# Performance work log

Measured on AMD Instinct MI355X. Metric: run time of the kernel, lower is better.

## Reference

```python
import jax, jax.numpy as jnp
import numpy as np

N = 16_777_216
H, W = 239, 319            # shape=(320,240): H=shape[1]-1, W=shape[0]-1
TIME_DIV = 4               # group_num=8 // 2
PSH, PSW = 16, 16          # patch_size
PH, PW = (H + 1) // PSH, (W + 1) // PSW   # 15, 20
TOKEN_NUM = PH * PW        # 300
PATCH_SIZE = PSH * PSW     # 256
B = 1e-4
TOTAL = TIME_DIV * 2 * PATCH_SIZE * TOKEN_NUM  # index[0]*bins[0]


def setup_inputs() -> dict:
    key = jax.random.key(0)
    k1, k2, k3, k4 = jax.random.split(key, 4)
    # events: (t sorted ascending, x in [0,W), y in [0,H), polarity in {0,1})
    t = jnp.sort(jax.random.uniform(k1, (N,), minval=0.0, maxval=1e4))
    xs = jax.random.uniform(k2, (N,), minval=0.0, maxval=float(W))
    ys = jax.random.uniform(k3, (N,), minval=0.0, maxval=float(H))
    p = jax.random.randint(k4, (N,), 0, 2).astype(jnp.float32)
    x = jnp.stack([t, xs, ys, p], axis=1)  # [N, 4], no inf values
    return {"x": x}


def reference(x):
    # x: [N, 4] columns (t, x, y, polarity); assumed inf-free (torch filter is a no-op)
    w = (x[:, 3] != 2).astype(x.dtype)                       # polarity-valid weight
    t = x[:, 0]
    wt = (t - t[0]) / (t[-1] - t[0] + B)                     # normalized-time weight
    pos = (jnp.floor(x[:, 1] / (W / PW + B))
           + jnp.floor(x[:, 2] / (H / PH + B)) * PW)         # which patch
    tok = (jnp.floor(x[:, 1] % (W / PW + B))
           + jnp.floor(x[:, 2] % (H / PH + B)) * ((W + 1) // PW))  # within-patch index
    dtime = jnp.floor(TIME_DIV * (t - t[0]) / (t[-1] - t[0] + 1.0))
    # multi-index -> 1-D (index_mapping): clamp each dim to [0, bins[d]] then ravel
    bins = jnp.array([TIME_DIV, 2, PATCH_SIZE, TOKEN_NUM], dtype=jnp.int32)
    index = jnp.array([2 * PATCH_SIZE * TOKEN_NUM, PATCH_SIZE * TOKEN_NUM,
                       TOKEN_NUM, 1], dtype=jnp.int32)
    x_nd = jnp.stack([dtime, x[:, 3], tok, pos]).astype(jnp.int32)  # [4, N]
    y_cl = jnp.clip(x_nd, 0, bins[:, None])
    l = jnp.sum(index[:, None] * y_cl, axis=0)                # [N] flat indices
    # two weighted histograms sharing the same indices (torch.bincount x2)
    h_w = jax.ops.segment_sum(w, l, num_segments=TOTAL).reshape(TIME_DIV, 2, PATCH_SIZE, TOKEN_NUM)
    h_wt = jax.ops.segment_sum(wt, l, num_segments=TOTAL).reshape(TIME_DIV, 2, PATCH_SIZE, TOKEN_NUM)
    y = jnp.stack([h_w, h_wt], axis=2)                        # [T, 2, 2, Patch, Token]
    return y.reshape(1, -1, PH, PW)
```

## Files before the change

### kernel.cpp

```cpp
#include <hip/hip_runtime.h>
#include <stdint.h>


#define TPB 256
#define B1 8192
#define CHUNK 2048
#define EVT (CHUNK / TPB)
#define NBUCKET 2400
#define SCAN_PER 10
#define GACC 16
#define NG (NBUCKET / GACC)
#define SLICES 16
#define RPS (B1 / SLICES)
#define HCELLS (GACC * 256)
#define ATPB 512
#define OUT_CH_STRIDE 76800
#define OUT_DP_STRIDE 153600

__device__ __forceinline__ void classify_full(const float4 e, const float t0,
                                              const float d_wt, const float d_dt,
                                              int& bucket, int& tok, float& wt) {
    const float c1 = (float)(319.0 / 20.0 + 1e-4);
    const float c2 = (float)(239.0 / 15.0 + 1e-4);
    const int pos = (int)(floorf(e.y / c1) + floorf(e.z / c2) * 20.0f);
    tok = (int)(floorf(fmodf(e.y, c1)) + floorf(fmodf(e.z, c2)) * 16.0f);
    const int dt = (int)floorf(4.0f * (e.x - t0) / d_dt);
    const int p  = (int)e.w;
    bucket = (dt * 2 + p) * 300 + pos;
    wt = (e.x - t0) / d_wt;
}

__global__ __launch_bounds__(TPB) void k_bin(const float4* __restrict__ x,
                                             uint32_t* __restrict__ payload,
                                             uint16_t* __restrict__ pfx,
                                             int n) {
    __shared__ uint32_t stage[CHUNK];
    __shared__ uint32_t cnt[NBUCKET];
    __shared__ uint32_t wsum[TPB / 64];

    for (int i = threadIdx.x; i < NBUCKET; i += TPB) cnt[i] = 0;
    __syncthreads();

    const float* xf = (const float*)x;
    const float t0 = xf[0];
    const float tlast = xf[(size_t)(n - 1) * 4];
    const float d_wt = tlast - t0 + 1e-4f;
    const float d_dt = tlast - t0 + 1.0f;

    const int beg = blockIdx.x * CHUNK;
    const bool full = (beg + CHUNK <= n);

    uint32_t pk[EVT];
    uint32_t bk[EVT];
    if (full) {
        #pragma unroll
        for (int k = 0; k < EVT; ++k) {
            float4 e = x[beg + threadIdx.x + k * TPB];
            int bucket, tok; float wt;
            classify_full(e, t0, d_wt, d_dt, bucket, tok, wt);
            uint32_t q = (uint32_t)(wt * 1048576.0f);
            q = q > 1048575u ? 1048575u : q;
            pk[k] = ((uint32_t)tok << 24) | ((uint32_t)(bucket & 15) << 20) | q;
            uint32_t rank = atomicAdd(&cnt[bucket], 1u);
            bk[k] = (uint32_t)bucket | (rank << 12);
        }
    } else {
        #pragma unroll
        for (int k = 0; k < EVT; ++k) {
            const int i = beg + threadIdx.x + k * TPB;
            if (i < n) {
                float4 e = x[i];
                int bucket, tok; float wt;
                classify_full(e, t0, d_wt, d_dt, bucket, tok, wt);
                uint32_t q = (uint32_t)(wt * 1048576.0f);
                q = q > 1048575u ? 1048575u : q;
                pk[k] = ((uint32_t)tok << 24) | ((uint32_t)(bucket & 15) << 20) | q;
                uint32_t rank = atomicAdd(&cnt[bucket], 1u);
                bk[k] = (uint32_t)bucket | (rank << 12);
            } else {
                bk[k] = 0xFFFFFFFFu;
            }
        }
    }
    __syncthreads();

    uint32_t v[SCAN_PER];
    uint32_t sum = 0;
    const int base_i = threadIdx.x * SCAN_PER;
    #pragma unroll
    for (int j = 0; j < SCAN_PER; ++j) {
        int idx = base_i + j;
        uint32_t c = (idx < NBUCKET) ? cnt[idx] : 0u;
        v[j] = sum;
        sum += c;
    }
    uint32_t inc = sum;
    #pragma unroll
    for (int off = 1; off < 64; off <<= 1) {
        uint32_t u = __shfl_up(inc, off, 64);
        if ((threadIdx.x & 63) >= off) inc += u;
    }
    const int wid = threadIdx.x >> 6, lid = threadIdx.x & 63;
    if (lid == 63) wsum[wid] = inc;
    __syncthreads();
    uint32_t woff = 0;
    for (int w = 0; w < wid; ++w) woff += wsum[w];
    const uint32_t excl = woff + inc - sum;

    uint16_t* prow = pfx + (size_t)blockIdx.x * NG;
    #pragma unroll
    for (int j = 0; j < SCAN_PER; ++j) {
        int idx = base_i + j;
        if (idx < NBUCKET) {
            uint32_t p = excl + v[j];
            cnt[idx] = p;
            if ((idx & 15) == 0) prow[idx >> 4] = (uint16_t)p;
        }
    }
    __syncthreads();

    if (full) {
        #pragma unroll
        for (int k = 0; k < EVT; ++k)
            stage[cnt[bk[k] & 0xFFFu] + (bk[k] >> 12)] = pk[k];
    } else {
        #pragma unroll
        for (int k = 0; k < EVT; ++k)
            if (bk[k] != 0xFFFFFFFFu)
                stage[cnt[bk[k] & 0xFFFu] + (bk[k] >> 12)] = pk[k];
    }
    __syncthreads();

    const int end = min(beg + CHUNK, n);
    const int cntE = end > beg ? end - beg : 0;
    uint32_t* pbase = payload + (size_t)blockIdx.x * CHUNK;
    const int n4 = cntE >> 2;
    const uint4* s4 = (const uint4*)stage;
    uint4* g4 = (uint4*)pbase;
    for (int i = threadIdx.x; i < n4; i += TPB) g4[i] = s4[i];
    for (int i = (n4 << 2) + threadIdx.x; i < cntE; i += TPB) pbase[i] = stage[i];
}

__global__ __launch_bounds__(256) void k_transpose(const uint16_t* __restrict__ in,
                                                   uint16_t* __restrict__ out) {
    __shared__ uint16_t tile[32][33];
    const int c0 = blockIdx.x * 32;
    const int r0 = blockIdx.y * 32;
    const int tx = threadIdx.x & 31;
    const int ty = threadIdx.x >> 5;
    for (int j = ty; j < 32; j += 8)
        if (c0 + tx < NG)
            tile[j][tx] = in[(size_t)(r0 + j) * NG + (c0 + tx)];
    __syncthreads();
    for (int j = ty; j < 32; j += 8)
        if (c0 + j < NG)
            out[(size_t)(c0 + j) * B1 + (r0 + tx)] = tile[tx][j];
}

__global__ __launch_bounds__(ATPB) void k_accum(const uint32_t* __restrict__ payload,
                                                const uint16_t* __restrict__ pfxT,
                                                unsigned long long* __restrict__ partial,
                                                int n) {
    const int g = blockIdx.x % NG;
    const int s = blockIdx.x / NG;

    __shared__ unsigned long long hist[HCELLS];
    for (int i = threadIdx.x; i < HCELLS; i += ATPB) hist[i] = 0ULL;
    __syncthreads();

    const uint16_t* colb = pfxT + (size_t)g * B1;
    const bool last = (g == NG - 1);
    const uint16_t* cole = colb + B1;

    const int wid = threadIdx.x >> 6, lid = threadIdx.x & 63;
    const int r0 = s * RPS + wid * 64;

    const int row = r0 + lid;
    uint32_t vb = colb[row];
    uint32_t ve;
    if (!last) {
        ve = cole[row];
    } else {
        int rc = n - row * CHUNK;
        ve = rc < 0 ? 0 : (rc > CHUNK ? CHUNK : rc);
    }

    const int q4 = lid >> 4;
    const int ql = lid & 15;
    for (int r = 0; r < 64; r += 4) {
        const int rr = r + q4;
        const uint32_t sb = __shfl(vb, rr, 64);
        const uint32_t se = __shfl(ve, rr, 64);
        const uint32_t* seg = payload + (size_t)(r0 + rr) * CHUNK;
        for (uint32_t j = sb + ql; j < se; j += 16) {
            const uint32_t w = seg[j];
            atomicAdd(&hist[w >> 20],
                      (1ULL << 40) | (unsigned long long)(w & 0xFFFFFu));
        }
    }
    __syncthreads();

    unsigned long long* pp = partial + ((size_t)s * NG + g) * HCELLS;
    for (int i = threadIdx.x; i < HCELLS; i += ATPB) pp[i] = hist[i];
}

__global__ __launch_bounds__(256) void k_out(const unsigned long long* __restrict__ partial,
                                             float* __restrict__ out) {
    const int i = blockIdx.x * 256 + threadIdx.x;
    unsigned long long v = 0ULL;
    #pragma unroll
    for (int s = 0; s < SLICES; ++s)
        v += partial[(size_t)s * (NG * HCELLS) + i];
    const int g = i >> 12;
    const int idx = i & 4095;
    const int tok = idx >> 4;
    const int c = idx & 15;
    const int b = g * GACC + c;
    const int pos = b % 300;
    const int dp = b / 300;
    const float cntf = (float)(uint32_t)(v >> 40);
    const float wts  = (float)(v & ((1ULL << 40) - 1)) * (1.0f / 1048576.0f);
    const int base0 = dp * OUT_DP_STRIDE + tok * 300 + pos;
    out[base0] = cntf;
    out[base0 + OUT_CH_STRIDE] = wts;
}

__global__ __launch_bounds__(TPB) void e2src_hist_atomic(const float4* __restrict__ x,
                                                         float* __restrict__ out, int n) {
    const float* xf = (const float*)x;
    const float t0 = xf[0];
    const float tlast = xf[(size_t)(n - 1) * 4];
    const float d_wt = tlast - t0 + 1e-4f;
    const float d_dt = tlast - t0 + 1.0f;
    int i = blockIdx.x * blockDim.x + threadIdx.x;
    const int stride = gridDim.x * blockDim.x;
    for (; i < n; i += stride) {
        float4 e = x[i];
        int bucket, tok; float wt;
        classify_full(e, t0, d_wt, d_dt, bucket, tok, wt);
        const int dp = bucket / 300, pos = bucket % 300;
        const int base = dp * OUT_DP_STRIDE + tok * 300 + pos;
        unsafeAtomicAdd(out + base, 1.0f);
        unsafeAtomicAdd(out + base + OUT_CH_STRIDE, wt);
    }
}

extern "C" void kernel_launch(void* const* d_in, const int* in_sizes, int n_in,
                              void* d_out, int out_size, void* d_ws, size_t ws_size,
                              hipStream_t stream) {
    const float* x = (const float*)d_in[0];
    float* out = (float*)d_out;
    const int n = in_sizes[0] / 4;

    const size_t payload_bytes = ((size_t)n * 4u + 7u) & ~(size_t)7u;
    const size_t pfx_bytes = (size_t)B1 * NG * 2u;
    const size_t part_bytes = (size_t)SLICES * NG * HCELLS * 8u;
    const size_t need = payload_bytes + 2u * pfx_bytes + part_bytes;

    if (ws_size < need || n > B1 * CHUNK || n <= 0) {
        hipMemsetAsync(d_out, 0, (size_t)out_size * sizeof(float), stream);
        if (n > 0)
            hipLaunchKernelGGL(e2src_hist_atomic, dim3(8192), dim3(TPB), 0, stream,
                               (const float4*)x, out, n);
        return;
    }

    uint32_t* payload = (uint32_t*)d_ws;
    uint16_t* pfx  = (uint16_t*)((char*)d_ws + payload_bytes);
    uint16_t* pfxT = (uint16_t*)((char*)d_ws + payload_bytes + pfx_bytes);
    unsigned long long* partial =
        (unsigned long long*)((char*)d_ws + payload_bytes + 2u * pfx_bytes);

    hipLaunchKernelGGL(k_bin, dim3(B1), dim3(TPB), 0, stream,
                       (const float4*)x, payload, pfx, n);
    hipLaunchKernelGGL(k_transpose, dim3((NG + 31) / 32, B1 / 32), dim3(256), 0,
                       stream, pfx, pfxT);
    hipLaunchKernelGGL(k_accum, dim3(NG * SLICES), dim3(ATPB), 0, stream,
                       payload, pfxT, partial, n);
    hipLaunchKernelGGL(k_out, dim3((NG * HCELLS) / 256), dim3(256), 0, stream,
                       partial, out);
}
```

Measured before the change: 442.4 us.

## Fuse prefix transpose into binning kernel and enlarge chunks, halve slices

The binning kernel now writes its per-group prefix offsets straight into the transposed layout, so the separate transpose kernel and its extra buffer go away. Chunk size doubles to 4096 events per block with half as many blocks. Accumulation slices drop from 16 to 8, which halves the partial-histogram buffer that the final reduction kernel must read. The accumulation block mapping is reordered so the slices of one group run in adjacent blocks. The trade-offs are scattered 2-byte strided stores in the binning kernel, more register and shared-memory pressure per block, and more work per accumulation block.

Result: slower. 452.7 us (+2.3%).

```diff
diff --git a/kernel.cpp b/kernel.cpp
--- a/kernel.cpp
+++ b/kernel.cpp
@@ -3,14 +3,14 @@
 
 
 #define TPB 256
-#define B1 8192
-#define CHUNK 2048
+#define B1 4096
+#define CHUNK 4096
 #define EVT (CHUNK / TPB)
 #define NBUCKET 2400
 #define SCAN_PER 10
 #define GACC 16
 #define NG (NBUCKET / GACC)
-#define SLICES 16
+#define SLICES 8
 #define RPS (B1 / SLICES)
 #define HCELLS (GACC * 256)
 #define ATPB 512
@@ -32,7 +32,7 @@
 
 __global__ __launch_bounds__(TPB) void k_bin(const float4* __restrict__ x,
                                              uint32_t* __restrict__ payload,
-                                             uint16_t* __restrict__ pfx,
+                                             uint16_t* __restrict__ pfxT,
                                              int n) {
     __shared__ uint32_t stage[CHUNK];
     __shared__ uint32_t cnt[NBUCKET];
@@ -107,14 +107,14 @@
     for (int w = 0; w < wid; ++w) woff += wsum[w];
     const uint32_t excl = woff + inc - sum;
 
-    uint16_t* prow = pfx + (size_t)blockIdx.x * NG;
     #pragma unroll
     for (int j = 0; j < SCAN_PER; ++j) {
         int idx = base_i + j;
         if (idx < NBUCKET) {
             uint32_t p = excl + v[j];
             cnt[idx] = p;
-            if ((idx & 15) == 0) prow[idx >> 4] = (uint16_t)p;
+            if ((idx & 15) == 0)
+                pfxT[(size_t)(idx >> 4) * B1 + blockIdx.x] = (uint16_t)p;
         }
     }
     __syncthreads();
@@ -141,28 +141,12 @@
     for (int i = (n4 << 2) + threadIdx.x; i < cntE; i += TPB) pbase[i] = stage[i];
 }
 
-__global__ __launch_bounds__(256) void k_transpose(const uint16_t* __restrict__ in,
-                                                   uint16_t* __restrict__ out) {
-    __shared__ uint16_t tile[32][33];
-    const int c0 = blockIdx.x * 32;
-    const int r0 = blockIdx.y * 32;
-    const int tx = threadIdx.x & 31;
-    const int ty = threadIdx.x >> 5;
-    for (int j = ty; j < 32; j += 8)
-        if (c0 + tx < NG)
-            tile[j][tx] = in[(size_t)(r0 + j) * NG + (c0 + tx)];
-    __syncthreads();
-    for (int j = ty; j < 32; j += 8)
-        if (c0 + j < NG)
-            out[(size_t)(c0 + j) * B1 + (r0 + tx)] = tile[tx][j];
-}
-
 __global__ __launch_bounds__(ATPB) void k_accum(const uint32_t* __restrict__ payload,
                                                 const uint16_t* __restrict__ pfxT,
                                                 unsigned long long* __restrict__ partial,
                                                 int n) {
-    const int g = blockIdx.x % NG;
-    const int s = blockIdx.x / NG;
+    const int g = blockIdx.x >> 3;
+    const int s = blockIdx.x & 7;
 
     __shared__ unsigned long long hist[HCELLS];
     for (int i = threadIdx.x; i < HCELLS; i += ATPB) hist[i] = 0ULL;
@@ -255,7 +239,7 @@
     const size_t payload_bytes = ((size_t)n * 4u + 7u) & ~(size_t)7u;
     const size_t pfx_bytes = (size_t)B1 * NG * 2u;
     const size_t part_bytes = (size_t)SLICES * NG * HCELLS * 8u;
-    const size_t need = payload_bytes + 2u * pfx_bytes + part_bytes;
+    const size_t need = payload_bytes + pfx_bytes + part_bytes;
 
     if (ws_size < need || n > B1 * CHUNK || n <= 0) {
         hipMemsetAsync(d_out, 0, (size_t)out_size * sizeof(float), stream);
@@ -266,15 +250,12 @@
     }
 
     uint32_t* payload = (uint32_t*)d_ws;
-    uint16_t* pfx  = (uint16_t*)((char*)d_ws + payload_bytes);
-    uint16_t* pfxT = (uint16_t*)((char*)d_ws + payload_bytes + pfx_bytes);
+    uint16_t* pfxT = (uint16_t*)((char*)d_ws + payload_bytes);
     unsigned long long* partial =
-        (unsigned long long*)((char*)d_ws + payload_bytes + 2u * pfx_bytes);
+        (unsigned long long*)((char*)d_ws + payload_bytes + pfx_bytes);
 
     hipLaunchKernelGGL(k_bin, dim3(B1), dim3(TPB), 0, stream,
-                       (const float4*)x, payload, pfx, n);
-    hipLaunchKernelGGL(k_transpose, dim3((NG + 31) / 32, B1 / 32), dim3(256), 0,
-                       stream, pfx, pfxT);
+                       (const float4*)x, payload, pfxT, n);
     hipLaunchKernelGGL(k_accum, dim3(NG * SLICES), dim3(ATPB), 0, stream,
                        payload, pfxT, partial, n);
     hipLaunchKernelGGL(k_out, dim3((NG * HCELLS) / 256), dim3(256), 0, stream,
```
